# Kernel tuning notes

Measured on AMD Instinct MI355X. Metric: run time of the kernel, lower is better.

The kernel has to match this reference:

```python
import jax, jax.numpy as jnp
import numpy as np

D_MODEL = 2048
N_HEADS = 16
KV_HEADS = 4
HEAD_DIM = D_MODEL // N_HEADS  # 128
GROUP = N_HEADS // KV_HEADS    # 4
B, T = 2, 2048
KV_WIDTH = KV_HEADS * HEAD_DIM


def _alibi_bias(n_heads: int, t: int) -> jnp.ndarray:
    # standard alibi slopes: geometric sequence 2^(-8i/n)
    slopes = 2.0 ** (-8.0 * (np.arange(1, n_heads + 1) / n_heads))
    rel = np.arange(t)[None, :] - np.arange(t)[:, None]  # j - i (<=0 in causal region)
    bias = slopes[:, None, None] * rel[None, :, :]
    return jnp.asarray(bias[None], dtype=jnp.float32)  # [1, H, T, T]


def setup_inputs() -> dict:
    key = jax.random.key(0)
    ks = jax.random.split(key, 5)
    s = 0.02
    x = jax.random.normal(ks[0], (B, T, D_MODEL), dtype=jnp.float32)
    attn_mask = jnp.tril(jnp.ones((T, T), dtype=bool))[None, None]  # [1,1,T,T]
    alibi_bias = _alibi_bias(N_HEADS, T)
    qkv_w = jax.random.normal(ks[1], (D_MODEL + 2 * KV_WIDTH, D_MODEL), dtype=jnp.float32) * s
    qkv_b = jax.random.normal(ks[2], (D_MODEL + 2 * KV_WIDTH,), dtype=jnp.float32) * s
    proj_w = jax.random.normal(ks[3], (D_MODEL, D_MODEL), dtype=jnp.float32) * s
    proj_b = jax.random.normal(ks[4], (D_MODEL,), dtype=jnp.float32) * s
    return {"x": x, "attn_mask": attn_mask, "alibi_bias": alibi_bias,
            "qkv_w": qkv_w, "qkv_b": qkv_b, "proj_w": proj_w, "proj_b": proj_b}


def reference(x, attn_mask, alibi_bias, qkv_w, qkv_b, proj_w, proj_b):
    b, t, c = x.shape
    qkv = x @ qkv_w.T + qkv_b  # [b, t, d + 2*kv_width]
    q = qkv[..., :D_MODEL]
    k = qkv[..., D_MODEL:D_MODEL + KV_WIDTH]
    v = qkv[..., D_MODEL + KV_WIDTH:]
    # grouped layout: query heads [b, kv, group, t, hd]; kv heads [b, kv, t, hd]
    q = q.reshape(b, t, KV_HEADS, GROUP, HEAD_DIM).transpose(0, 2, 3, 1, 4)
    k = k.reshape(b, t, KV_HEADS, HEAD_DIM).transpose(0, 2, 1, 3)
    v = v.reshape(b, t, KV_HEADS, HEAD_DIM).transpose(0, 2, 1, 3)
    scale = 1.0 / jnp.sqrt(jnp.asarray(HEAD_DIM, x.dtype))
    att = jnp.einsum('bkgtd,bksd->bkgts', q, k) * scale  # [b, kv, group, t, t]
    att = att + alibi_bias.reshape(1, KV_HEADS, GROUP, t, t)
    att = jnp.where(attn_mask[:, :, None], att, jnp.asarray(-jnp.inf, att.dtype))
    att = jax.nn.softmax(att, axis=-1)
    out = jnp.einsum('bkgts,bksd->bkgtd', att, v)  # [b, kv, group, t, hd]
    out = out.transpose(0, 3, 1, 2, 4).reshape(b, t, c)
    return out @ proj_w.T + proj_b
```

## Files before the change

kernel.cpp:

```cpp
#include <hip/hip_runtime.h>
#include <hip/hip_bf16.h>
#include <math.h>

typedef unsigned short u16;
typedef unsigned int   u32;
typedef __attribute__((ext_vector_type(8))) short bf16x8;
typedef __attribute__((ext_vector_type(4))) float f32x4;
typedef __attribute__((ext_vector_type(4))) unsigned short u16x4;
typedef __attribute__((ext_vector_type(4))) unsigned int   u32x4;

#define T_SEQ 2048
#define BATCH 2
#define NHEAD 16
#define KVHEADS 4
#define HD 128
#define DM 2048
#define QKV_N 3072
#define MROWS 4096

__device__ __forceinline__ float bf2f(u16 u) {
    union { u32 i; float f; } v; v.i = ((u32)u) << 16; return v.f;
}
__device__ __forceinline__ u16 f2bf(float f) {
    u32 x = __float_as_uint(f);
    u32 r = (x + 0x7fffu + ((x >> 16) & 1u)) >> 16;
    return (u16)r;
}

__device__ __forceinline__ void gl16(const void* g, void* lds) {
    __builtin_amdgcn_global_load_lds(
        (const __attribute__((address_space(1))) void*)g,
        (__attribute__((address_space(3))) void*)lds, 16, 0, 0);
}

__device__ __forceinline__ int alibi_w1(int h) {
    return (int)(36.0f * exp2f(0.5f * (float)(h + 1)) * (1.0f / 64.0f)) + 2;
}

__global__ void reset_u32(u32* p, u32 v) { *p = v; }

__global__ void cvt_f32_bf16(const float* __restrict__ in, u16* __restrict__ out, int nq)
{
    int i = blockIdx.x * blockDim.x + threadIdx.x;
    const int stride = gridDim.x * blockDim.x;
    for (; i < nq; i += stride) {
        f32x4 v = ((const f32x4*)in)[i];
        u16x4 o = { f2bf(v[0]), f2bf(v[1]), f2bf(v[2]), f2bf(v[3]) };
        ((u16x4*)out)[i] = o;
    }
}

template <int EPI>
__global__ __launch_bounds__(256, 3)
void gemm_bt(const u16* __restrict__ A, const u16* __restrict__ Bw,
             const float* __restrict__ bias, u16* __restrict__ C,
             float* __restrict__ Cf, u16* __restrict__ Vt, int M, int N, int K)
{
    __shared__ __align__(16) u16 As[128 * 64];
    __shared__ __align__(16) u16 Bs[128 * 64];

    const int tid = threadIdx.x;
    const int l = tid & 63;
    const int w = tid >> 6;
    const int wr = w >> 1, wc = w & 1;
    const int bm = blockIdx.x, bn = blockIdx.y;

    const int lrow = l >> 3;
    const int lsl  = (l & 7) ^ lrow;
    const size_t aBase = (size_t)(bm * 128 + w * 8 + lrow) * K + lsl * 8;
    const size_t bBase = (size_t)(bn * 128 + w * 8 + lrow) * K + lsl * 8;

    const int sw = (l & 7) << 4;
    int offA[4], offB[4];
#pragma unroll
    for (int mf = 0; mf < 4; ++mf)
        offA[mf] = (wr * 64 + mf * 16 + (l & 15)) * 128 + (((l >> 4) * 16) ^ sw);
#pragma unroll
    for (int nf = 0; nf < 4; ++nf)
        offB[nf] = (wc * 64 + nf * 16 + (l & 15)) * 128 + (((l >> 4) * 16) ^ sw);

    f32x4 acc[4][4];
#pragma unroll
    for (int i = 0; i < 4; ++i)
#pragma unroll
        for (int j = 0; j < 4; ++j)
            acc[i][j] = (f32x4){0.f, 0.f, 0.f, 0.f};

    const int nK = K >> 6;
    for (int kt = 0; kt < nK; ++kt) {
        __syncthreads();
#pragma unroll
        for (int j = 0; j < 4; ++j) {
            gl16(A  + aBase + (size_t)j * 32 * K + kt * 64,
                 (char*)As + (w * 8 + j * 32) * 128);
            gl16(Bw + bBase + (size_t)j * 32 * K + kt * 64,
                 (char*)Bs + (w * 8 + j * 32) * 128);
        }
        __syncthreads();
#pragma unroll
        for (int kk = 0; kk < 2; ++kk) {
            bf16x8 af[4], bfr[4];
#pragma unroll
            for (int mf = 0; mf < 4; ++mf)
                af[mf] = *(const bf16x8*)((const char*)As + (offA[mf] ^ (kk << 6)));
#pragma unroll
            for (int nf = 0; nf < 4; ++nf)
                bfr[nf] = *(const bf16x8*)((const char*)Bs + (offB[nf] ^ (kk << 6)));
            __builtin_amdgcn_s_setprio(1);
#pragma unroll
            for (int mf = 0; mf < 4; ++mf)
#pragma unroll
                for (int nf = 0; nf < 4; ++nf)
                    acc[mf][nf] = __builtin_amdgcn_mfma_f32_16x16x32_bf16(
                        af[mf], bfr[nf], acc[mf][nf], 0, 0, 0);
            __builtin_amdgcn_s_setprio(0);
        }
    }

    const int row0 = bm * 128 + wr * 64 + ((l >> 4) << 2);
    const int col0 = bn * 128 + wc * 64 + (l & 15);
#pragma unroll
    for (int mf = 0; mf < 4; ++mf) {
#pragma unroll
        for (int nf = 0; nf < 4; ++nf) {
            const int row = row0 + mf * 16;
            const int col = col0 + nf * 16;
            const float bv = bias[col];
            float v0 = acc[mf][nf][0] + bv;
            float v1 = acc[mf][nf][1] + bv;
            float v2 = acc[mf][nf][2] + bv;
            float v3 = acc[mf][nf][3] + bv;
            if (EPI == 0) {
                if (col < 2560) {
                    C[(size_t)(row + 0) * QKV_N + col] = f2bf(v0);
                    C[(size_t)(row + 1) * QKV_N + col] = f2bf(v1);
                    C[(size_t)(row + 2) * QKV_N + col] = f2bf(v2);
                    C[(size_t)(row + 3) * QKV_N + col] = f2bf(v3);
                } else {
                    const int dd = col - 2560;
                    const int kv = dd >> 7;
                    const int d = dd & 127;
                    const int bidx = row >> 11;
                    const int tt = row & 2047;
                    u16x4 pv = {f2bf(v0), f2bf(v1), f2bf(v2), f2bf(v3)};
                    *(u16x4*)(Vt + ((size_t)((bidx * KVHEADS + kv) * HD + d)) * T_SEQ + tt) = pv;
                }
            } else {
                Cf[(size_t)(row + 0) * DM + col] = v0;
                Cf[(size_t)(row + 1) * DM + col] = v1;
                Cf[(size_t)(row + 2) * DM + col] = v2;
                Cf[(size_t)(row + 3) * DM + col] = v3;
            }
        }
    }
}

#define PWS_SEG 8448
__global__ __launch_bounds__(256, 2)
void attn_fwd(const u16* __restrict__ qkv, const u16* __restrict__ Vt,
              u16* __restrict__ AO, u32* __restrict__ ctr,
              float* __restrict__ PWS)
{
    __shared__ __align__(16) u16 Ks[2 * 64 * 128];
    __shared__ __align__(16) u16 Vs[2 * 64 * 128];
    __shared__ __align__(16) u16 Ps[4 * 16 * 64];
    __shared__ int sh_item;

    const int tid = threadIdx.x;
    const int l = tid & 63;
    const int w = tid >> 6;

    const int sw = (l & 7) << 4;
    int offK0[4];
#pragma unroll
    for (int nf = 0; nf < 4; ++nf)
        offK0[nf] = (nf * 16 + (l & 15)) * 256 + (((l >> 4) * 16) ^ sw);

    const int rk = tid >> 4, skk = tid & 15;
    const int loK = rk * 256 + ((skk * 16) ^ ((rk & 7) << 4));
    const int rv = tid >> 3, svv = tid & 7;
    const int loV = rv * 128 + ((svv * 16) ^ ((rv & 7) << 4));

    const float LOG2E = 1.4426950408889634f;
    const float scale2 = 0.08838834764831845f * LOG2E;
    const bf16x8 ones = {(short)0x3F80, (short)0x3F80, (short)0x3F80, (short)0x3F80,
                         (short)0x3F80, (short)0x3F80, (short)0x3F80, (short)0x3F80};

    int item = blockIdx.x;

    for (;;) {
        __syncthreads();
        if (item < 0 && tid == 0) sh_item = (int)atomicAdd(ctr, 1u);
        __syncthreads();
        if (item < 0) item = sh_item;
        if (item >= 1536) break;

        int seg, qt, bh;
        if (item < 512)       { seg = 0; qt = 31 - (item >> 5);          bh = item & 31; }
        else if (item < 1024) { seg = 1; qt = 31 - ((item - 512) >> 5);  bh = item & 31; }
        else                  { seg = 0; qt = 15 - ((item - 1024) >> 5); bh = item & 31; }
        const int b = bh >> 4;
        const int h = bh & 15;
        const int kvh = h >> 2;
        const int q0 = qt << 6;

        const float slope2 = exp2f(-0.5f * (float)(h + 1)) * LOG2E;
        const int W1 = alibi_w1(h);
        const int jt_min = (qt - W1 > 0) ? (qt - W1) : 0;
        const bool split = (qt >= 16) && (W1 >= 16);
        if (seg == 1 && !split) { item = -1; continue; }

        const int jt_hi = seg ? (qt - 16) : qt;
        const int jt_lo = seg ? jt_min : (split ? (qt - 15) : jt_min);

        const size_t gK0 = (size_t)(b * T_SEQ + rk) * QKV_N + 2048 + kvh * HD + skk * 8;
        const size_t gV0 = (size_t)((b * KVHEADS + kvh) * HD + rv) * T_SEQ + svv * 8;

        const size_t qrow_off = (size_t)h * HD + ((l >> 4) << 3);
        bf16x8 qreg[4];
#pragma unroll
        for (int kk = 0; kk < 4; ++kk)
            qreg[kk] = *(const bf16x8*)(qkv +
                (size_t)(b * T_SEQ + q0 + w * 16 + (l & 15)) * QKV_N + qrow_off + kk * 32);

        float m_run[4];
        f32x4 o[8];
        f32x4 lacc = (f32x4){0.f, 0.f, 0.f, 0.f};
#pragma unroll
        for (int i = 0; i < 4; ++i) m_run[i] = -1e30f;
#pragma unroll
        for (int nf = 0; nf < 8; ++nf) o[nf] = (f32x4){0.f, 0.f, 0.f, 0.f};

        const int tb = q0 + w * 16 + ((l >> 4) << 2);
        const float dslope = slope2 * 64.0f;
        float abase[4][4];
#pragma unroll
        for (int nf = 0; nf < 4; ++nf)
#pragma unroll
            for (int i = 0; i < 4; ++i)
                abase[nf][i] = slope2 * (float)((jt_hi << 6) + nf * 16 + (l & 15) - (tb + i));

        u32x4 pk[4], pv[4];
#pragma unroll
        for (int j = 0; j < 4; ++j) {
            pk[j] = *(const u32x4*)(qkv + gK0 + (size_t)((jt_hi << 6) + j * 16) * QKV_N);
            pv[j] = *(const u32x4*)(Vt + gV0 + (jt_hi << 6) + (size_t)j * 32 * T_SEQ);
        }
#pragma unroll
        for (int j = 0; j < 4; ++j) {
            *(u32x4*)((char*)Ks + loK + j * 16 * 256) = pk[j];
            *(u32x4*)((char*)Vs + loV + j * 32 * 128) = pv[j];
        }

        for (int c = 0, jt = jt_hi; jt >= jt_lo; --jt, ++c) {
            const int bsel = (c & 1) << 14;

            __syncthreads();

            if (jt > jt_lo) {
                const int ns0 = (jt - 1) << 6;
#pragma unroll
                for (int j = 0; j < 4; ++j) {
                    pk[j] = *(const u32x4*)(qkv + gK0 + (size_t)(ns0 + j * 16) * QKV_N);
                    pv[j] = *(const u32x4*)(Vt + gV0 + ns0 + (size_t)j * 32 * T_SEQ);
                }
            }

            f32x4 sc[4];
#pragma unroll
            for (int nf = 0; nf < 4; ++nf) sc[nf] = (f32x4){0.f, 0.f, 0.f, 0.f};
            __builtin_amdgcn_s_setprio(1);
#pragma unroll
            for (int kk = 0; kk < 4; ++kk) {
#pragma unroll
                for (int nf = 0; nf < 4; ++nf) {
                    bf16x8 kb = *(const bf16x8*)((const char*)Ks + bsel + (offK0[nf] ^ (kk << 6)));
                    sc[nf] = __builtin_amdgcn_mfma_f32_16x16x32_bf16(qreg[kk], kb, sc[nf], 0, 0, 0);
                }
            }
            __builtin_amdgcn_s_setprio(0);

            float vals[4][4];
#pragma unroll
            for (int nf = 0; nf < 4; ++nf)
#pragma unroll
                for (int i = 0; i < 4; ++i) {
                    vals[nf][i] = fmaf(sc[nf][i], scale2, abase[nf][i]);
                    abase[nf][i] -= dslope;
                }
            if (seg == 0 && c == 0) {
                const int s0 = jt << 6;
#pragma unroll
                for (int nf = 0; nf < 4; ++nf) {
                    const int scol = s0 + nf * 16 + (l & 15);
#pragma unroll
                    for (int i = 0; i < 4; ++i)
                        if (scol > tb + i) vals[nf][i] = -__builtin_inff();
                }
            }

            float lm[4];
#pragma unroll
            for (int i = 0; i < 4; ++i)
                lm[i] = fmaxf(fmaxf(vals[0][i], vals[1][i]), fmaxf(vals[2][i], vals[3][i]));
            const bool ok = (lm[0] <= m_run[0] + 10.f) && (lm[1] <= m_run[1] + 10.f) &&
                            (lm[2] <= m_run[2] + 10.f) && (lm[3] <= m_run[3] + 10.f);
            if (!__all(ok)) {
                float corr[4];
#pragma unroll
                for (int i = 0; i < 4; ++i) {
                    float mx = lm[i];
#pragma unroll
                    for (int d = 1; d < 16; d <<= 1) mx = fmaxf(mx, __shfl_xor(mx, d, 64));
                    const float mn = fmaxf(m_run[i], mx);
                    corr[i] = exp2f(m_run[i] - mn);
                    m_run[i] = mn;
                }
#pragma unroll
                for (int nf = 0; nf < 8; ++nf) {
                    o[nf][0] *= corr[0]; o[nf][1] *= corr[1];
                    o[nf][2] *= corr[2]; o[nf][3] *= corr[3];
                }
                lacc[0] *= corr[0]; lacc[1] *= corr[1];
                lacc[2] *= corr[2]; lacc[3] *= corr[3];
            }

            const int pbase = w * 2048;
#pragma unroll
            for (int nf = 0; nf < 4; ++nf)
#pragma unroll
                for (int i = 0; i < 4; ++i) {
                    const float p = exp2f(vals[nf][i] - m_run[i]);
                    const int r = ((l >> 4) << 2) + i;
                    const int off = pbase + ((r * 128 + nf * 32 + ((l & 15) << 1)) ^ ((r & 7) << 4));
                    *(u16*)((char*)Ps + off) = f2bf(p);
                }

            const int rp = l & 15;
            __builtin_amdgcn_s_setprio(1);
#pragma unroll
            for (int kk = 0; kk < 2; ++kk) {
                bf16x8 pfr = *(const bf16x8*)((const char*)Ps + pbase +
                              (rp * 128 + ((((l >> 4) * 16) ^ sw) ^ (kk << 6))));
                lacc = __builtin_amdgcn_mfma_f32_16x16x32_bf16(pfr, ones, lacc, 0, 0, 0);
#pragma unroll
                for (int nf = 0; nf < 8; ++nf) {
                    const int offv = (nf * 16 + (l & 15)) * 128 + ((((l >> 4) * 16) ^ sw) ^ (kk << 6));
                    bf16x8 vb = *(const bf16x8*)((const char*)Vs + bsel + offv);
                    o[nf] = __builtin_amdgcn_mfma_f32_16x16x32_bf16(pfr, vb, o[nf], 0, 0, 0);
                }
            }
            __builtin_amdgcn_s_setprio(0);

            if (jt > jt_lo) {
                const int b2 = ((c + 1) & 1) << 14;
#pragma unroll
                for (int j = 0; j < 4; ++j) {
                    *(u32x4*)((char*)Ks + b2 + loK + j * 16 * 256) = pk[j];
                    *(u32x4*)((char*)Vs + b2 + loV + j * 32 * 128) = pv[j];
                }
            }
        }

        if (!split) {
            float rinv[4];
#pragma unroll
            for (int i = 0; i < 4; ++i) rinv[i] = 1.f / lacc[i];
            const size_t orow = (size_t)(b * T_SEQ + q0 + w * 16 + ((l >> 4) << 2));
#pragma unroll
            for (int nf = 0; nf < 8; ++nf) {
                const int col = h * HD + nf * 16 + (l & 15);
#pragma unroll
                for (int i = 0; i < 4; ++i)
                    AO[(orow + i) * DM + col] = f2bf(o[nf][i] * rinv[i]);
            }
        } else {
            const int rid = (bh << 5) | qt;
            float* base = PWS + (size_t)(rid * 2 + seg) * PWS_SEG;
            const int row0 = w * 16 + ((l >> 4) << 2);
#pragma unroll
            for (int nf = 0; nf < 8; ++nf) {
                const int col = nf * 16 + (l & 15);
#pragma unroll
                for (int i = 0; i < 4; ++i)
                    base[(row0 + i) * 128 + col] = o[nf][i];
            }
            if ((l & 15) == 0) {
#pragma unroll
                for (int i = 0; i < 4; ++i) {
                    base[8192 + row0 + i] = m_run[i];
                    base[8256 + row0 + i] = lacc[i];
                }
            }
        }

        item = -1;
    }
}

__global__ __launch_bounds__(256)
void attn_combine(const float* __restrict__ PWS, u16* __restrict__ AO)
{
    const int rid = blockIdx.x;
    const int qt = rid & 31;
    const int bh = rid >> 5;
    const int b = bh >> 4;
    const int h = bh & 15;
    if (!(qt >= 16 && alibi_w1(h) >= 16)) return;

    const float* p0 = PWS + (size_t)(rid * 2 + 0) * PWS_SEG;
    const float* p1 = PWS + (size_t)(rid * 2 + 1) * PWS_SEG;

    const int t = threadIdx.x;
    const int row = t >> 2;
    const int c0 = (t & 3) * 32;

    const float m0 = p0[8192 + row], m1 = p1[8192 + row];
    const float l0 = p0[8256 + row], l1 = p1[8256 + row];
    const float m = fmaxf(m0, m1);
    const float w0 = exp2f(m0 - m), w1 = exp2f(m1 - m);
    const float rinv = 1.f / (l0 * w0 + l1 * w1);

    const size_t ao = (size_t)(b * T_SEQ + (qt << 6) + row) * DM + h * HD + c0;
#pragma unroll
    for (int j = 0; j < 32; ++j) {
        const float v = (p0[row * 128 + c0 + j] * w0 + p1[row * 128 + c0 + j] * w1) * rinv;
        AO[ao + j] = f2bf(v);
    }
}

extern "C" void kernel_launch(void* const* d_in, const int* in_sizes, int n_in,
                              void* d_out, int out_size, void* d_ws, size_t ws_size,
                              hipStream_t stream)
{
    const float* x      = (const float*)d_in[0];
    const float* qkv_w  = (const float*)d_in[3];
    const float* qkv_b  = (const float*)d_in[4];
    const float* proj_w = (const float*)d_in[5];
    const float* proj_b = (const float*)d_in[6];
    float* out = (float*)d_out;

    u16* ws  = (u16*)d_ws;
    u16* xb  = ws;
    u16* AO  = ws;
    u16* qwb = ws + 8388608;
    u16* pwb = qwb + 6291456;
    u16* qkv = pwb + 4194304;
    u16* Vt  = qkv + 12582912;
    u32* ctr = (u32*)(ws + 33554432);
    float* PWS = (float*)((char*)d_ws + 67108880);

    reset_u32<<<1, 1, 0, stream>>>(ctr, 512u);
    cvt_f32_bf16<<<2048, 256, 0, stream>>>(x,      xb,  8388608 / 4);
    cvt_f32_bf16<<<2048, 256, 0, stream>>>(qkv_w,  qwb, 6291456 / 4);
    cvt_f32_bf16<<<1024, 256, 0, stream>>>(proj_w, pwb, 4194304 / 4);

    gemm_bt<0><<<dim3(32, 24), 256, 0, stream>>>(xb, qwb, qkv_b, qkv, nullptr, Vt,
                                                 MROWS, QKV_N, DM);
    attn_fwd<<<dim3(512), 256, 0, stream>>>(qkv, Vt, AO, ctr, PWS);
    attn_combine<<<dim3(1024), 256, 0, stream>>>(PWS, AO);
    gemm_bt<1><<<dim3(32, 16), 256, 0, stream>>>(AO, pwb, proj_b, nullptr, out, nullptr,
                                                 MROWS, DM, DM);
}
```

Measured before the change: 187.6 us.

## Process 128-row query tiles per block so each K/V tile feeds two MFMA rows

The attention kernel now handles 128 query rows per work item, with each wave owning 32 rows as two 16-row MFMA fragments. Each K and V fragment loaded from LDS is reused for both fragments, which halves K/V LDS and global traffic per query row and halves the number of work items. The split into two segments now depends on the tile count, and waves whose first tile is fully masked skip it. The cost is higher register pressure from doubled accumulators at two blocks per CU, plus a larger P buffer and partial-sum workspace.

```diff
diff --git a/kernel.cpp b/kernel.cpp
--- a/kernel.cpp
+++ b/kernel.cpp
@@ -155,7 +155,7 @@
     }
 }
 
-#define PWS_SEG 8448
+#define PWS_SEG2 16640
 __global__ __launch_bounds__(256, 2)
 void attn_fwd(const u16* __restrict__ qkv, const u16* __restrict__ Vt,
               u16* __restrict__ AO, u32* __restrict__ ctr,
@@ -163,7 +163,7 @@
 {
     __shared__ __align__(16) u16 Ks[2 * 64 * 128];
     __shared__ __align__(16) u16 Vs[2 * 64 * 128];
-    __shared__ __align__(16) u16 Ps[4 * 16 * 64];
+    __shared__ __align__(16) u16 Ps[4 * 32 * 64];
     __shared__ int sh_item;
 
     const int tid = threadIdx.x;
@@ -171,10 +171,13 @@
     const int w = tid >> 6;
 
     const int sw = (l & 7) << 4;
-    int offK0[4];
+    int offK0[4], offV0[8];
 #pragma unroll
     for (int nf = 0; nf < 4; ++nf)
         offK0[nf] = (nf * 16 + (l & 15)) * 256 + (((l >> 4) * 16) ^ sw);
+#pragma unroll
+    for (int nf = 0; nf < 8; ++nf)
+        offV0[nf] = (nf * 16 + (l & 15)) * 128 + (((l >> 4) * 16) ^ sw);
 
     const int rk = tid >> 4, skk = tid & 15;
     const int loK = rk * 256 + ((skk * 16) ^ ((rk & 7) << 4));
@@ -193,52 +196,62 @@
         if (item < 0 && tid == 0) sh_item = (int)atomicAdd(ctr, 1u);
         __syncthreads();
         if (item < 0) item = sh_item;
-        if (item >= 1536) break;
-
-        int seg, qt, bh;
-        if (item < 512)       { seg = 0; qt = 31 - (item >> 5);          bh = item & 31; }
-        else if (item < 1024) { seg = 1; qt = 31 - ((item - 512) >> 5);  bh = item & 31; }
-        else                  { seg = 0; qt = 15 - ((item - 1024) >> 5); bh = item & 31; }
+        if (item >= 1024) break;
+
+        const int seg = (item < 512) ? 0 : 1;
+        const int idx = (item < 512) ? item : item - 512;
+        const int qt2 = 15 - (idx >> 5);
+        const int bh = idx & 31;
         const int b = bh >> 4;
         const int h = bh & 15;
         const int kvh = h >> 2;
-        const int q0 = qt << 6;
+        const int q0 = qt2 << 7;
 
         const float slope2 = exp2f(-0.5f * (float)(h + 1)) * LOG2E;
         const int W1 = alibi_w1(h);
-        const int jt_min = (qt - W1 > 0) ? (qt - W1) : 0;
-        const bool split = (qt >= 16) && (W1 >= 16);
+        const int jt_min = (2 * qt2 - W1 > 0) ? (2 * qt2 - W1) : 0;
+        const int ntiles = 2 * qt2 + 2 - jt_min;
+        const bool split = (ntiles >= 20);
         if (seg == 1 && !split) { item = -1; continue; }
 
-        const int jt_hi = seg ? (qt - 16) : qt;
-        const int jt_lo = seg ? jt_min : (split ? (qt - 15) : jt_min);
+        int jt_hi, jt_lo;
+        if (!split)        { jt_hi = 2 * qt2 + 1;          jt_lo = jt_min; }
+        else if (seg == 0) { jt_hi = 2 * qt2 + 1;          jt_lo = jt_min + (ntiles >> 1); }
+        else               { jt_hi = jt_min + (ntiles >> 1) - 1; jt_lo = jt_min; }
 
         const size_t gK0 = (size_t)(b * T_SEQ + rk) * QKV_N + 2048 + kvh * HD + skk * 8;
         const size_t gV0 = (size_t)((b * KVHEADS + kvh) * HD + rv) * T_SEQ + svv * 8;
 
-        const size_t qrow_off = (size_t)h * HD + ((l >> 4) << 3);
-        bf16x8 qreg[4];
-#pragma unroll
-        for (int kk = 0; kk < 4; ++kk)
-            qreg[kk] = *(const bf16x8*)(qkv +
-                (size_t)(b * T_SEQ + q0 + w * 16 + (l & 15)) * QKV_N + qrow_off + kk * 32);
-
-        float m_run[4];
-        f32x4 o[8];
-        f32x4 lacc = (f32x4){0.f, 0.f, 0.f, 0.f};
-#pragma unroll
-        for (int i = 0; i < 4; ++i) m_run[i] = -1e30f;
-#pragma unroll
-        for (int nf = 0; nf < 8; ++nf) o[nf] = (f32x4){0.f, 0.f, 0.f, 0.f};
-
-        const int tb = q0 + w * 16 + ((l >> 4) << 2);
+        bf16x8 qreg[2][4];
+#pragma unroll
+        for (int mf = 0; mf < 2; ++mf)
+#pragma unroll
+            for (int kk = 0; kk < 4; ++kk)
+                qreg[mf][kk] = *(const bf16x8*)(qkv +
+                    (size_t)(b * T_SEQ + q0 + w * 32 + mf * 16 + (l & 15)) * QKV_N +
+                    (size_t)h * HD + kk * 32 + ((l >> 4) << 3));
+
+        float m_run[2][4];
+        f32x4 o[2][8];
+        f32x4 lacc[2] = {(f32x4){0.f,0.f,0.f,0.f}, (f32x4){0.f,0.f,0.f,0.f}};
+#pragma unroll
+        for (int mf = 0; mf < 2; ++mf) {
+#pragma unroll
+            for (int i = 0; i < 4; ++i) m_run[mf][i] = -1e30f;
+#pragma unroll
+            for (int nf = 0; nf < 8; ++nf) o[mf][nf] = (f32x4){0.f, 0.f, 0.f, 0.f};
+        }
+
         const float dslope = slope2 * 64.0f;
-        float abase[4][4];
-#pragma unroll
-        for (int nf = 0; nf < 4; ++nf)
+        float rowoff[2][4], coloff[4];
+#pragma unroll
+        for (int mf = 0; mf < 2; ++mf)
 #pragma unroll
             for (int i = 0; i < 4; ++i)
-                abase[nf][i] = slope2 * (float)((jt_hi << 6) + nf * 16 + (l & 15) - (tb + i));
+                rowoff[mf][i] = slope2 * (float)((jt_hi << 6) + (l & 15)
+                                - (q0 + w * 32 + mf * 16 + ((l >> 4) << 2) + i));
+#pragma unroll
+        for (int nf = 0; nf < 4; ++nf) coloff[nf] = slope2 * (float)(nf * 16);
 
         u32x4 pk[4], pv[4];
 #pragma unroll
@@ -266,91 +279,126 @@
                 }
             }
 
-            f32x4 sc[4];
-#pragma unroll
-            for (int nf = 0; nf < 4; ++nf) sc[nf] = (f32x4){0.f, 0.f, 0.f, 0.f};
-            __builtin_amdgcn_s_setprio(1);
-#pragma unroll
-            for (int kk = 0; kk < 4; ++kk) {
-#pragma unroll
-                for (int nf = 0; nf < 4; ++nf) {
-                    bf16x8 kb = *(const bf16x8*)((const char*)Ks + bsel + (offK0[nf] ^ (kk << 6)));
-                    sc[nf] = __builtin_amdgcn_mfma_f32_16x16x32_bf16(qreg[kk], kb, sc[nf], 0, 0, 0);
-                }
+            const bool skipw = (seg == 0 && c == 0 && w < 2);
+            if (!skipw) {
+                f32x4 sc[2][4];
+#pragma unroll
+                for (int mf = 0; mf < 2; ++mf)
+#pragma unroll
+                    for (int nf = 0; nf < 4; ++nf) sc[mf][nf] = (f32x4){0.f,0.f,0.f,0.f};
+                __builtin_amdgcn_s_setprio(1);
+#pragma unroll
+                for (int kk = 0; kk < 4; ++kk) {
+#pragma unroll
+                    for (int nf = 0; nf < 4; ++nf) {
+                        bf16x8 kb = *(const bf16x8*)((const char*)Ks + bsel + (offK0[nf] ^ (kk << 6)));
+                        sc[0][nf] = __builtin_amdgcn_mfma_f32_16x16x32_bf16(qreg[0][kk], kb, sc[0][nf], 0, 0, 0);
+                        sc[1][nf] = __builtin_amdgcn_mfma_f32_16x16x32_bf16(qreg[1][kk], kb, sc[1][nf], 0, 0, 0);
+                    }
+                }
+                __builtin_amdgcn_s_setprio(0);
+
+                float vals[2][4][4];
+#pragma unroll
+                for (int mf = 0; mf < 2; ++mf)
+#pragma unroll
+                    for (int nf = 0; nf < 4; ++nf)
+#pragma unroll
+                        for (int i = 0; i < 4; ++i)
+                            vals[mf][nf][i] = fmaf(sc[mf][nf][i], scale2,
+                                                   rowoff[mf][i] + coloff[nf]);
+                if (seg == 0 && c < 2) {
+                    const bool needmask = (c == 0) ? (w >= 2) : (w < 2);
+                    if (needmask) {
+                        const int s0i = jt << 6;
+#pragma unroll
+                        for (int mf = 0; mf < 2; ++mf)
+#pragma unroll
+                            for (int nf = 0; nf < 4; ++nf) {
+                                const int scol = s0i + nf * 16 + (l & 15);
+#pragma unroll
+                                for (int i = 0; i < 4; ++i) {
+                                    const int trow = q0 + w * 32 + mf * 16 + ((l >> 4) << 2) + i;
+                                    if (scol > trow) vals[mf][nf][i] = -__builtin_inff();
+                                }
+                            }
+                    }
+                }
+
+                float lm[2][4];
+                bool ok = true;
+#pragma unroll
+                for (int mf = 0; mf < 2; ++mf)
+#pragma unroll
+                    for (int i = 0; i < 4; ++i) {
+                        lm[mf][i] = fmaxf(fmaxf(vals[mf][0][i], vals[mf][1][i]),
+                                          fmaxf(vals[mf][2][i], vals[mf][3][i]));
+                        ok = ok && (lm[mf][i] <= m_run[mf][i] + 10.f);
+                    }
+                if (!__all(ok)) {
+                    float corr[2][4];
+#pragma unroll
+                    for (int mf = 0; mf < 2; ++mf)
+#pragma unroll
+                        for (int i = 0; i < 4; ++i) {
+                            float mx = lm[mf][i];
+#pragma unroll
+                            for (int d = 1; d < 16; d <<= 1) mx = fmaxf(mx, __shfl_xor(mx, d, 64));
+                            const float mn = fmaxf(m_run[mf][i], mx);
+                            corr[mf][i] = exp2f(m_run[mf][i] - mn);
+                            m_run[mf][i] = mn;
+                        }
+#pragma unroll
+                    for (int mf = 0; mf < 2; ++mf) {
+#pragma unroll
+                        for (int nf = 0; nf < 8; ++nf) {
+                            o[mf][nf][0] *= corr[mf][0]; o[mf][nf][1] *= corr[mf][1];
+                            o[mf][nf][2] *= corr[mf][2]; o[mf][nf][3] *= corr[mf][3];
+                        }
+                        lacc[mf][0] *= corr[mf][0]; lacc[mf][1] *= corr[mf][1];
+                        lacc[mf][2] *= corr[mf][2]; lacc[mf][3] *= corr[mf][3];
+                    }
+                }
+
+                const int pbase = w * 4096;
+#pragma unroll
+                for (int mf = 0; mf < 2; ++mf)
+#pragma unroll
+                    for (int nf = 0; nf < 4; ++nf)
+#pragma unroll
+                        for (int i = 0; i < 4; ++i) {
+                            const float p = exp2f(vals[mf][nf][i] - m_run[mf][i]);
+                            const int r = mf * 16 + ((l >> 4) << 2) + i;
+                            const int off = pbase + ((r * 128 + nf * 32 + ((l & 15) << 1))
+                                            ^ ((r & 7) << 4));
+                            *(u16*)((char*)Ps + off) = f2bf(p);
+                        }
+
+                __builtin_amdgcn_s_setprio(1);
+#pragma unroll
+                for (int kk = 0; kk < 2; ++kk) {
+                    bf16x8 pfr[2];
+#pragma unroll
+                    for (int mf = 0; mf < 2; ++mf) {
+                        const int rp = mf * 16 + (l & 15);
+                        pfr[mf] = *(const bf16x8*)((const char*)Ps + pbase +
+                                   (rp * 128 + ((((l >> 4) * 16) ^ sw) ^ (kk << 6))));
+                        lacc[mf] = __builtin_amdgcn_mfma_f32_16x16x32_bf16(pfr[mf], ones, lacc[mf], 0, 0, 0);
+                    }
+#pragma unroll
+                    for (int nf = 0; nf < 8; ++nf) {
+                        bf16x8 vb = *(const bf16x8*)((const char*)Vs + bsel + (offV0[nf] ^ (kk << 6)));
+                        o[0][nf] = __builtin_amdgcn_mfma_f32_16x16x32_bf16(pfr[0], vb, o[0][nf], 0, 0, 0);
+                        o[1][nf] = __builtin_amdgcn_mfma_f32_16x16x32_bf16(pfr[1], vb, o[1][nf], 0, 0, 0);
+                    }
+                }
+                __builtin_amdgcn_s_setprio(0);
             }
-            __builtin_amdgcn_s_setprio(0);
-
-            float vals[4][4];
-#pragma unroll
-            for (int nf = 0; nf < 4; ++nf)
-#pragma unroll
-                for (int i = 0; i < 4; ++i) {
-                    vals[nf][i] = fmaf(sc[nf][i], scale2, abase[nf][i]);
-                    abase[nf][i] -= dslope;
-                }
-            if (seg == 0 && c == 0) {
-                const int s0 = jt << 6;
-#pragma unroll
-                for (int nf = 0; nf < 4; ++nf) {
-                    const int scol = s0 + nf * 16 + (l & 15);
-#pragma unroll
-                    for (int i = 0; i < 4; ++i)
-                        if (scol > tb + i) vals[nf][i] = -__builtin_inff();
-                }
-            }
-
-            float lm[4];
-#pragma unroll
-            for (int i = 0; i < 4; ++i)
-                lm[i] = fmaxf(fmaxf(vals[0][i], vals[1][i]), fmaxf(vals[2][i], vals[3][i]));
-            const bool ok = (lm[0] <= m_run[0] + 10.f) && (lm[1] <= m_run[1] + 10.f) &&
-                            (lm[2] <= m_run[2] + 10.f) && (lm[3] <= m_run[3] + 10.f);
-            if (!__all(ok)) {
-                float corr[4];
-#pragma unroll
-                for (int i = 0; i < 4; ++i) {
-                    float mx = lm[i];
-#pragma unroll
-                    for (int d = 1; d < 16; d <<= 1) mx = fmaxf(mx, __shfl_xor(mx, d, 64));
-                    const float mn = fmaxf(m_run[i], mx);
-                    corr[i] = exp2f(m_run[i] - mn);
-                    m_run[i] = mn;
-                }
-#pragma unroll
-                for (int nf = 0; nf < 8; ++nf) {
-                    o[nf][0] *= corr[0]; o[nf][1] *= corr[1];
-                    o[nf][2] *= corr[2]; o[nf][3] *= corr[3];
-                }
-                lacc[0] *= corr[0]; lacc[1] *= corr[1];
-                lacc[2] *= corr[2]; lacc[3] *= corr[3];
-            }
-
-            const int pbase = w * 2048;
-#pragma unroll
-            for (int nf = 0; nf < 4; ++nf)
-#pragma unroll
-                for (int i = 0; i < 4; ++i) {
-                    const float p = exp2f(vals[nf][i] - m_run[i]);
-                    const int r = ((l >> 4) << 2) + i;
-                    const int off = pbase + ((r * 128 + nf * 32 + ((l & 15) << 1)) ^ ((r & 7) << 4));
-                    *(u16*)((char*)Ps + off) = f2bf(p);
-                }
-
-            const int rp = l & 15;
-            __builtin_amdgcn_s_setprio(1);
-#pragma unroll
-            for (int kk = 0; kk < 2; ++kk) {
-                bf16x8 pfr = *(const bf16x8*)((const char*)Ps + pbase +
-                              (rp * 128 + ((((l >> 4) * 16) ^ sw) ^ (kk << 6))));
-                lacc = __builtin_amdgcn_mfma_f32_16x16x32_bf16(pfr, ones, lacc, 0, 0, 0);
-#pragma unroll
-                for (int nf = 0; nf < 8; ++nf) {
-                    const int offv = (nf * 16 + (l & 15)) * 128 + ((((l >> 4) * 16) ^ sw) ^ (kk << 6));
-                    bf16x8 vb = *(const bf16x8*)((const char*)Vs + bsel + offv);
-                    o[nf] = __builtin_amdgcn_mfma_f32_16x16x32_bf16(pfr, vb, o[nf], 0, 0, 0);
-                }
-            }
-            __builtin_amdgcn_s_setprio(0);
+
+#pragma unroll
+            for (int mf = 0; mf < 2; ++mf)
+#pragma unroll
+                for (int i = 0; i < 4; ++i) rowoff[mf][i] -= dslope;
 
             if (jt > jt_lo) {
                 const int b2 = ((c + 1) & 1) << 14;
@@ -363,33 +411,39 @@
         }
 
         if (!split) {
-            float rinv[4];
-#pragma unroll
-            for (int i = 0; i < 4; ++i) rinv[i] = 1.f / lacc[i];
-            const size_t orow = (size_t)(b * T_SEQ + q0 + w * 16 + ((l >> 4) << 2));
-#pragma unroll
-            for (int nf = 0; nf < 8; ++nf) {
-                const int col = h * HD + nf * 16 + (l & 15);
-#pragma unroll
-                for (int i = 0; i < 4; ++i)
-                    AO[(orow + i) * DM + col] = f2bf(o[nf][i] * rinv[i]);
+#pragma unroll
+            for (int mf = 0; mf < 2; ++mf) {
+                float rinv[4];
+#pragma unroll
+                for (int i = 0; i < 4; ++i) rinv[i] = 1.f / lacc[mf][i];
+                const size_t orow = (size_t)(b * T_SEQ + q0 + w * 32 + mf * 16 + ((l >> 4) << 2));
+#pragma unroll
+                for (int nf = 0; nf < 8; ++nf) {
+                    const int col = h * HD + nf * 16 + (l & 15);
+#pragma unroll
+                    for (int i = 0; i < 4; ++i)
+                        AO[(orow + i) * DM + col] = f2bf(o[mf][nf][i] * rinv[i]);
+                }
             }
         } else {
-            const int rid = (bh << 5) | qt;
-            float* base = PWS + (size_t)(rid * 2 + seg) * PWS_SEG;
-            const int row0 = w * 16 + ((l >> 4) << 2);
-#pragma unroll
-            for (int nf = 0; nf < 8; ++nf) {
-                const int col = nf * 16 + (l & 15);
-#pragma unroll
-                for (int i = 0; i < 4; ++i)
-                    base[(row0 + i) * 128 + col] = o[nf][i];
-            }
-            if ((l & 15) == 0) {
-#pragma unroll
-                for (int i = 0; i < 4; ++i) {
-                    base[8192 + row0 + i] = m_run[i];
-                    base[8256 + row0 + i] = lacc[i];
+            const int rid = (bh << 4) | qt2;
+            float* base = PWS + (size_t)(rid * 2 + seg) * PWS_SEG2;
+#pragma unroll
+            for (int mf = 0; mf < 2; ++mf) {
+                const int row0 = w * 32 + mf * 16 + ((l >> 4) << 2);
+#pragma unroll
+                for (int nf = 0; nf < 8; ++nf) {
+                    const int col = nf * 16 + (l & 15);
+#pragma unroll
+                    for (int i = 0; i < 4; ++i)
+                        base[(row0 + i) * 128 + col] = o[mf][nf][i];
+                }
+                if ((l & 15) == 0) {
+#pragma unroll
+                    for (int i = 0; i < 4; ++i) {
+                        base[16384 + row0 + i] = m_run[mf][i];
+                        base[16512 + row0 + i] = lacc[mf][i];
+                    }
                 }
             }
         }
@@ -402,30 +456,35 @@
 void attn_combine(const float* __restrict__ PWS, u16* __restrict__ AO)
 {
     const int rid = blockIdx.x;
-    const int qt = rid & 31;
-    const int bh = rid >> 5;
+    const int qt2 = rid & 15;
+    const int bh = rid >> 4;
     const int b = bh >> 4;
     const int h = bh & 15;
-    if (!(qt >= 16 && alibi_w1(h) >= 16)) return;
-
-    const float* p0 = PWS + (size_t)(rid * 2 + 0) * PWS_SEG;
-    const float* p1 = PWS + (size_t)(rid * 2 + 1) * PWS_SEG;
+    const int W1 = alibi_w1(h);
+    const int jt_min = (2 * qt2 - W1 > 0) ? (2 * qt2 - W1) : 0;
+    if (2 * qt2 + 2 - jt_min < 20) return;
+
+    const float* p0 = PWS + (size_t)(rid * 2 + 0) * PWS_SEG2;
+    const float* p1 = PWS + (size_t)(rid * 2 + 1) * PWS_SEG2;
 
     const int t = threadIdx.x;
-    const int row = t >> 2;
-    const int c0 = (t & 3) * 32;
-
-    const float m0 = p0[8192 + row], m1 = p1[8192 + row];
-    const float l0 = p0[8256 + row], l1 = p1[8256 + row];
+    const int row = t >> 1;
+    const int c0 = (t & 1) * 64;
+
+    const float m0 = p0[16384 + row], m1 = p1[16384 + row];
+    const float l0 = p0[16512 + row], l1 = p1[16512 + row];
     const float m = fmaxf(m0, m1);
     const float w0 = exp2f(m0 - m), w1 = exp2f(m1 - m);
     const float rinv = 1.f / (l0 * w0 + l1 * w1);
 
-    const size_t ao = (size_t)(b * T_SEQ + (qt << 6) + row) * DM + h * HD + c0;
-#pragma unroll
-    for (int j = 0; j < 32; ++j) {
-        const float v = (p0[row * 128 + c0 + j] * w0 + p1[row * 128 + c0 + j] * w1) * rinv;
-        AO[ao + j] = f2bf(v);
+    const size_t ao = (size_t)(b * T_SEQ + (qt2 << 7) + row) * DM + h * HD + c0;
+#pragma unroll
+    for (int j = 0; j < 64; j += 4) {
+        f32x4 a = *(const f32x4*)(p0 + row * 128 + c0 + j);
+        f32x4 bx = *(const f32x4*)(p1 + row * 128 + c0 + j);
+#pragma unroll
+        for (int q = 0; q < 4; ++q)
+            AO[ao + j + q] = f2bf((a[q] * w0 + bx[q] * w1) * rinv);
     }
 }
 
@@ -458,7 +517,7 @@
     gemm_bt<0><<<dim3(32, 24), 256, 0, stream>>>(xb, qwb, qkv_b, qkv, nullptr, Vt,
                                                  MROWS, QKV_N, DM);
     attn_fwd<<<dim3(512), 256, 0, stream>>>(qkv, Vt, AO, ctr, PWS);
-    attn_combine<<<dim3(1024), 256, 0, stream>>>(PWS, AO);
+    attn_combine<<<dim3(512), 256, 0, stream>>>(PWS, AO);
     gemm_bt<1><<<dim3(32, 16), 256, 0, stream>>>(AO, pwb, proj_b, nullptr, out, nullptr,
                                                  MROWS, DM, DM);
 }
```

Result: slower. 252.6 us (+34.7%).

## Load K/V tiles directly from global memory into LDS, bypassing registers

Applied to the files above, without the earlier changes.

Replaces register-staged K/V prefetch (global load into VGPRs, then LDS store after the PV MMAs) with direct global-to-LDS 16-byte loads via gl16 into the double buffer. The per-lane row and slot mapping is rewritten so the XOR swizzle in LDS still matches the MFMA read offsets. This is meant to free the VGPRs held by the staging buffers and remove the LDS store instructions from the inner loop. In exchange, correctness now depends on the async loads being complete before the barrier at the top of the next iteration.

```diff
diff --git a/kernel.cpp b/kernel.cpp
--- a/kernel.cpp
+++ b/kernel.cpp
@@ -176,10 +176,9 @@
     for (int nf = 0; nf < 4; ++nf)
         offK0[nf] = (nf * 16 + (l & 15)) * 256 + (((l >> 4) * 16) ^ sw);
 
-    const int rk = tid >> 4, skk = tid & 15;
-    const int loK = rk * 256 + ((skk * 16) ^ ((rk & 7) << 4));
-    const int rv = tid >> 3, svv = tid & 7;
-    const int loV = rv * 128 + ((svv * 16) ^ ((rv & 7) << 4));
+    const int ldChunk = w * 1024;
+    const int kslot = ((l & 15) ^ ((4 * (w & 1)) | (l >> 4))) * 8;
+    const int vslot = ((l & 7) ^ (l >> 3)) * 8;
 
     const float LOG2E = 1.4426950408889634f;
     const float scale2 = 0.08838834764831845f * LOG2E;
@@ -213,8 +212,10 @@
         const int jt_hi = seg ? (qt - 16) : qt;
         const int jt_lo = seg ? jt_min : (split ? (qt - 15) : jt_min);
 
-        const size_t gK0 = (size_t)(b * T_SEQ + rk) * QKV_N + 2048 + kvh * HD + skk * 8;
-        const size_t gV0 = (size_t)((b * KVHEADS + kvh) * HD + rv) * T_SEQ + svv * 8;
+        const size_t gK0 = (size_t)(b * T_SEQ + 4 * w + (l >> 4)) * QKV_N
+                           + 2048 + kvh * HD + kslot;
+        const size_t gV0 = (size_t)((b * KVHEADS + kvh) * HD + 8 * w + (l >> 3)) * T_SEQ
+                           + vslot;
 
         const size_t qrow_off = (size_t)h * HD + ((l >> 4) << 3);
         bf16x8 qreg[4];
@@ -240,16 +241,12 @@
             for (int i = 0; i < 4; ++i)
                 abase[nf][i] = slope2 * (float)((jt_hi << 6) + nf * 16 + (l & 15) - (tb + i));
 
-        u32x4 pk[4], pv[4];
 #pragma unroll
         for (int j = 0; j < 4; ++j) {
-            pk[j] = *(const u32x4*)(qkv + gK0 + (size_t)((jt_hi << 6) + j * 16) * QKV_N);
-            pv[j] = *(const u32x4*)(Vt + gV0 + (jt_hi << 6) + (size_t)j * 32 * T_SEQ);
-        }
-#pragma unroll
-        for (int j = 0; j < 4; ++j) {
-            *(u32x4*)((char*)Ks + loK + j * 16 * 256) = pk[j];
-            *(u32x4*)((char*)Vs + loV + j * 32 * 128) = pv[j];
+            gl16(qkv + gK0 + (size_t)((jt_hi << 6) + 16 * j) * QKV_N,
+                 (char*)Ks + ldChunk + j * 4096);
+            gl16(Vt + gV0 + (size_t)(32 * j) * T_SEQ + (jt_hi << 6),
+                 (char*)Vs + ldChunk + j * 4096);
         }
 
         for (int c = 0, jt = jt_hi; jt >= jt_lo; --jt, ++c) {
@@ -259,10 +256,13 @@
 
             if (jt > jt_lo) {
                 const int ns0 = (jt - 1) << 6;
+                const int b2 = ((c + 1) & 1) << 14;
 #pragma unroll
                 for (int j = 0; j < 4; ++j) {
-                    pk[j] = *(const u32x4*)(qkv + gK0 + (size_t)(ns0 + j * 16) * QKV_N);
-                    pv[j] = *(const u32x4*)(Vt + gV0 + ns0 + (size_t)j * 32 * T_SEQ);
+                    gl16(qkv + gK0 + (size_t)(ns0 + 16 * j) * QKV_N,
+                         (char*)Ks + b2 + ldChunk + j * 4096);
+                    gl16(Vt + gV0 + (size_t)(32 * j) * T_SEQ + ns0,
+                         (char*)Vs + b2 + ldChunk + j * 4096);
                 }
             }
 
@@ -351,15 +351,6 @@
                 }
             }
             __builtin_amdgcn_s_setprio(0);
-
-            if (jt > jt_lo) {
-                const int b2 = ((c + 1) & 1) << 14;
-#pragma unroll
-                for (int j = 0; j < 4; ++j) {
-                    *(u32x4*)((char*)Ks + b2 + loK + j * 16 * 256) = pk[j];
-                    *(u32x4*)((char*)Vs + b2 + loV + j * 32 * 128) = pv[j];
-                }
-            }
         }
 
         if (!split) {
```

Result: slower. 193.6 us (+3.2%).
